# Kernel tuning notes

Measured on AMD Instinct MI355X. Metric: run time of the kernel, lower is better.

The kernel has to match this reference:

```python
import jax, jax.numpy as jnp
import numpy as np

N_NODES = 50000
IN_CH = 256
Z_DIM = 64
N_EDGES = 800000


def setup_inputs() -> dict:
    key = jax.random.key(0)
    k_x, k_e, k_wm, k_ws = jax.random.split(key, 4)
    x = jax.random.normal(k_x, (N_NODES, IN_CH), dtype=jnp.float32)
    edge_index = jax.random.randint(k_e, (2, N_EDGES), 0, N_NODES, dtype=jnp.int64)
    # Glorot-style init like PyG GCNConv
    scale = 1.0 / np.sqrt(IN_CH)
    W_mu = jax.random.uniform(k_wm, (IN_CH, Z_DIM), dtype=jnp.float32, minval=-scale, maxval=scale)
    W_logstd = jax.random.uniform(k_ws, (IN_CH, Z_DIM), dtype=jnp.float32, minval=-scale, maxval=scale)
    b_mu = jnp.zeros((Z_DIM,), dtype=jnp.float32)
    b_logstd = jnp.zeros((Z_DIM,), dtype=jnp.float32)
    return {"x": x, "edge_index": edge_index, "W_mu": W_mu, "b_mu": b_mu,
            "W_logstd": W_logstd, "b_logstd": b_logstd}


def _gcn_conv(x, W, b, src, dst, deg_inv_sqrt, num_nodes):
    # PyG GCNConv: out = D^{-1/2} (A + I) D^{-1/2} X W + b
    xw = x @ W                                   # [N, Z]
    norm = deg_inv_sqrt[src] * deg_inv_sqrt[dst]  # [E+N]
    msg = xw[src] * norm[:, None]                 # gather + scale, [E+N, Z]
    agg = jax.ops.segment_sum(msg, dst, num_segments=num_nodes)  # scatter-add
    return agg + b


def reference(x, edge_index, W_mu, b_mu, W_logstd, b_logstd):
    num_nodes = x.shape[0]
    loops = jnp.arange(num_nodes, dtype=edge_index.dtype)
    src = jnp.concatenate([edge_index[0], loops])
    dst = jnp.concatenate([edge_index[1], loops])
    # degree (with self loops) on target nodes, symmetric normalization
    deg = jax.ops.segment_sum(jnp.ones_like(dst, dtype=x.dtype), dst, num_segments=num_nodes)
    deg_inv_sqrt = jnp.where(deg > 0, jax.lax.rsqrt(jnp.maximum(deg, 1.0)), 0.0)
    mu = _gcn_conv(x, W_mu, b_mu, src, dst, deg_inv_sqrt, num_nodes)
    logstd = _gcn_conv(x, W_logstd, b_logstd, src, dst, deg_inv_sqrt, num_nodes)
    return (mu, logstd)
```

## Files before the change

### kernel.cpp

```cpp
#include <hip/hip_runtime.h>

#define N_NODES 50000
#define IN_CH   256
#define Z_DIM   64
#define N_EDGES 800000
#define CH2     128
#define NODE_OFF (N_NODES * Z_DIM)
#define NBLK    ((N_NODES + 255) / 256)
#define SEG     8
#define SEGN    50048
#define NBUCKET (SEG * SEGN)
#define CAP     16
#define ECHUNKS (N_EDGES / 256)
#define TM      128
#define GTILES  ((N_NODES + TM - 1) / TM)
#define NW      32768

typedef __bf16 bf16x8 __attribute__((ext_vector_type(8)));
typedef float  f32x4  __attribute__((ext_vector_type(4)));

__device__ __forceinline__ unsigned short f2bf(float f) {
    __bf16 h = (__bf16)f;
    unsigned short u;
    __builtin_memcpy(&u, &h, 2);
    return u;
}
__device__ __forceinline__ float bf_lo(unsigned w) { return __uint_as_float(w << 16); }
__device__ __forceinline__ float bf_hi(unsigned w) { return __uint_as_float(w & 0xFFFF0000u); }

__global__ void k_pre(int* __restrict__ cur8,
                      const float* __restrict__ Wmu, const float* __restrict__ Wls,
                      unsigned short* __restrict__ WbT) {
    int g = blockIdx.x * 256 + threadIdx.x;
    if (g < NBUCKET) cur8[g] = 0;
    int h = g - NBUCKET;
    if (h >= 0 && h < NW) {
        int n = h >> 8, k = h & 255;
        float v = (n < 64) ? Wmu[(size_t)k * 64 + n] : Wls[(size_t)k * 64 + (n - 64)];
        WbT[(size_t)n * 256 + k] = f2bf(v);
    }
}

__global__ __launch_bounds__(256) void k_scat(const int* __restrict__ src,
                                              const int* __restrict__ dst,
                                              int* __restrict__ cur8,
                                              unsigned short* __restrict__ pk2) {
    int e = blockIdx.x * 256 + threadIdx.x;
    int s = src[e];
    int d = dst[e];
    unsigned xcc;
    asm("s_getreg_b32 %0, hwreg(HW_REG_XCC_ID)" : "=s"(xcc));
    int idx = (int)(xcc & (SEG - 1)) * SEGN + d;
    int pos = __hip_atomic_fetch_add(&cur8[idx], 1, __ATOMIC_RELAXED,
                                     __HIP_MEMORY_SCOPE_WORKGROUP);
    if (pos < CAP) pk2[(size_t)idx * CAP + pos] = (unsigned short)s;
}

#define CSP2 136
__global__ __launch_bounds__(256, 2) void k_gemm(const float* __restrict__ x,
                                                 const unsigned short* __restrict__ WbT,
                                                 unsigned short* __restrict__ xwb) {
    __shared__ __align__(16) unsigned short As[TM * 256];
    const int tid = threadIdx.x;
    const int r0  = blockIdx.x * TM;

    {
        int row_l0 = tid >> 3;
        int cb     = (tid & 7) * 32;
#pragma unroll
        for (int r = 0; r < 4; ++r) {
            int row_l = r * 32 + row_l0;
            int row   = r0 + row_l;
            char* dpb = (char*)As + row_l * 512;
            unsigned cswz = (unsigned)((row_l & 7) << 4);
            if (row < N_NODES) {
                const float4* xp = (const float4*)(x + (size_t)row * IN_CH + cb);
#pragma unroll
                for (int i = 0; i < 4; ++i) {
                    float4 a = xp[2 * i];
                    float4 b = xp[2 * i + 1];
                    uint4 w;
                    w.x = (unsigned)f2bf(a.x) | ((unsigned)f2bf(a.y) << 16);
                    w.y = (unsigned)f2bf(a.z) | ((unsigned)f2bf(a.w) << 16);
                    w.z = (unsigned)f2bf(b.x) | ((unsigned)f2bf(b.y) << 16);
                    w.w = (unsigned)f2bf(b.z) | ((unsigned)f2bf(b.w) << 16);
                    *(uint4*)(dpb + (((unsigned)(cb * 2 + i * 16)) ^ cswz)) = w;
                }
            } else {
                uint4 z = make_uint4(0, 0, 0, 0);
#pragma unroll
                for (int i = 0; i < 4; ++i)
                    *(uint4*)(dpb + (((unsigned)(cb * 2 + i * 16)) ^ cswz)) = z;
            }
        }
    }
    __syncthreads();

    const int wv    = tid >> 6;
    const int lane  = tid & 63;
    const int m     = lane & 15;
    const int q     = lane >> 4;
    const int rbase = wv * 32;

    f32x4 acc[2][8] = {};
    const char* apb0 = (const char*)As + (rbase + m) * 512;
    const char* apb1 = apb0 + 16 * 512;
    const unsigned   sw  = (unsigned)((m & 7) << 4);
    const unsigned short* bp = WbT + (size_t)m * 256 + q * 8;

#pragma unroll
    for (int k0 = 0; k0 < IN_CH; k0 += 32) {
        unsigned off = ((unsigned)(q * 16 + 2 * k0)) ^ sw;
        bf16x8 a0 = *(const bf16x8*)(apb0 + off);
        bf16x8 a1 = *(const bf16x8*)(apb1 + off);
#pragma unroll
        for (int nt = 0; nt < 8; ++nt) {
            bf16x8 bf_ = *(const bf16x8*)(bp + (size_t)nt * 16 * 256 + k0);
            acc[0][nt] = __builtin_amdgcn_mfma_f32_16x16x32_bf16(a0, bf_, acc[0][nt], 0, 0, 0);
            acc[1][nt] = __builtin_amdgcn_mfma_f32_16x16x32_bf16(a1, bf_, acc[1][nt], 0, 0, 0);
        }
    }

    __syncthreads();
    {
        unsigned short* Css = As;
#pragma unroll
        for (int mi = 0; mi < 2; ++mi)
#pragma unroll
            for (int nt = 0; nt < 8; ++nt)
#pragma unroll
                for (int r = 0; r < 4; ++r)
                    Css[(rbase + mi * 16 + q * 4 + r) * CSP2 + nt * 16 + m] =
                        f2bf(acc[mi][nt][r]);
    }
    __syncthreads();
    {
        int row_l = tid >> 2;
        int c0    = (tid & 3) * 32;
#pragma unroll
        for (int rr = 0; rr < 2; ++rr) {
            int rl  = rr * 64 + row_l;
            int row = r0 + rl;
            if (row < N_NODES) {
                const uint4* cp = (const uint4*)(As + rl * CSP2 + c0);
                uint4 w0 = cp[0];
                uint4 w1 = cp[1];
                uint4 w2 = cp[2];
                uint4 w3 = cp[3];
                uint4* op = (uint4*)(xwb + (size_t)row * CH2 + c0);
                op[0] = w0; op[1] = w1; op[2] = w2; op[3] = w3;
            }
        }
    }
}

__global__ void k_dinv(const int* __restrict__ cur8, float* __restrict__ dinv) {
    int i = blockIdx.x * 256 + threadIdx.x;
    if (i >= N_NODES) return;
    int t = 1;
#pragma unroll
    for (int xg = 0; xg < SEG; ++xg) t += cur8[xg * SEGN + i];
    dinv[i] = rsqrtf((float)t);
}

#define PAIR(jj, pr)                                                          \
    if (2 * (jj) < cnt) {                                                     \
        int sa = (int)((pr) & 0xFFFFu);                                       \
        int sb = (int)((pr) >> 16);                                           \
        bool hb = (2 * (jj) + 1) < cnt;                                       \
        int sbe = hb ? sb : sa;                                               \
        float na = di * dinv[sa];                                             \
        float nb = hb ? di * dinv[sbe] : 0.f;                                 \
        const uint4 wa = *(const uint4*)(xwb + (size_t)sa * CH2 + cl * 8);    \
        const uint4 wb = *(const uint4*)(xwb + (size_t)sbe * CH2 + cl * 8);   \
        acc[0] += bf_lo(wa.x) * na + bf_lo(wb.x) * nb;                        \
        acc[1] += bf_hi(wa.x) * na + bf_hi(wb.x) * nb;                        \
        acc[2] += bf_lo(wa.y) * na + bf_lo(wb.y) * nb;                        \
        acc[3] += bf_hi(wa.y) * na + bf_hi(wb.y) * nb;                        \
        acc[4] += bf_lo(wa.z) * na + bf_lo(wb.z) * nb;                        \
        acc[5] += bf_hi(wa.z) * na + bf_hi(wb.z) * nb;                        \
        acc[6] += bf_lo(wa.w) * na + bf_lo(wb.w) * nb;                        \
        acc[7] += bf_hi(wa.w) * na + bf_hi(wb.w) * nb;                        \
    }

__global__ __launch_bounds__(256) void k_gather(const int* __restrict__ cur8,
                                                const unsigned short* __restrict__ pk2,
                                                const unsigned short* __restrict__ xwb,
                                                const float* __restrict__ dinv,
                                                const float* __restrict__ bmu,
                                                const float* __restrict__ bls,
                                                float* __restrict__ out) {
    const int i    = blockIdx.x * 4 + (threadIdx.x >> 6);
    const int lane = threadIdx.x & 63;
    const int q    = lane >> 4;
    const int cl   = lane & 15;

    float di = dinv[i];
    float acc[8] = {0.f, 0.f, 0.f, 0.f, 0.f, 0.f, 0.f, 0.f};
    if (q == 0) {
        float sq = di * di;
        uint4 w = *(const uint4*)(xwb + (size_t)i * CH2 + cl * 8);
        acc[0] = bf_lo(w.x) * sq; acc[1] = bf_hi(w.x) * sq;
        acc[2] = bf_lo(w.y) * sq; acc[3] = bf_hi(w.y) * sq;
        acc[4] = bf_lo(w.z) * sq; acc[5] = bf_hi(w.z) * sq;
        acc[6] = bf_lo(w.w) * sq; acc[7] = bf_hi(w.w) * sq;
    }

#pragma unroll
    for (int b = 0; b < 2; ++b) {
        const int idx = (q + b * 4) * SEGN + i;
        int cnt = cur8[idx];
        if (cnt > CAP) cnt = CAP;
        const uint4* pb = (const uint4*)(pk2 + (size_t)idx * CAP);
        const uint4 e0 = pb[0];
        const uint4 e1 = pb[1];
        PAIR(0, e0.x) PAIR(1, e0.y) PAIR(2, e0.z) PAIR(3, e0.w)
        PAIR(4, e1.x) PAIR(5, e1.y) PAIR(6, e1.z) PAIR(7, e1.w)
    }

#pragma unroll
    for (int k = 0; k < 8; ++k) {
        acc[k] += __shfl_xor(acc[k], 16);
        acc[k] += __shfl_xor(acc[k], 32);
    }

    if (lane < 16) {
        int c0 = cl * 8;
        const float* bb = (c0 < 64) ? (bmu + c0) : (bls + (c0 - 64));
        float4 b0 = *(const float4*)(bb + 0);
        float4 b1 = *(const float4*)(bb + 4);
        float* o = (c0 < 64) ? (out + (size_t)i * 64 + c0)
                             : (out + NODE_OFF + (size_t)i * 64 + (c0 - 64));
        *(float4*)(o + 0) = make_float4(acc[0] + b0.x, acc[1] + b0.y,
                                        acc[2] + b0.z, acc[3] + b0.w);
        *(float4*)(o + 4) = make_float4(acc[4] + b1.x, acc[5] + b1.y,
                                        acc[6] + b1.z, acc[7] + b1.w);
    }
}

extern "C" void kernel_launch(void* const* d_in, const int* in_sizes, int n_in,
                              void* d_out, int out_size, void* d_ws, size_t ws_size,
                              hipStream_t stream) {
    const float* x   = (const float*)d_in[0];
    const int*   ei  = (const int*)d_in[1];
    const float* Wmu = (const float*)d_in[2];
    const float* bmu = (const float*)d_in[3];
    const float* Wls = (const float*)d_in[4];
    const float* bls = (const float*)d_in[5];
    float* out = (float*)d_out;

    const int* src = ei;
    const int* dst = ei + N_EDGES;

    char* ws = (char*)d_ws;
    int*            cur8 = (int*)(ws + 0);
    float*          dinv = (float*)(ws + 1638400);
    unsigned short* WbT  = (unsigned short*)(ws + 1867776);
    unsigned short* pk2  = (unsigned short*)(ws + 2097152);
    unsigned short* xwb  = (unsigned short*)(ws + 16777216);

    k_pre<<<(NBUCKET + NW + 255) / 256, 256, 0, stream>>>(cur8, Wmu, Wls, WbT);
    k_scat<<<ECHUNKS, 256, 0, stream>>>(src, dst, cur8, pk2);
    k_gemm<<<GTILES, 256, 0, stream>>>(x, WbT, xwb);
    k_dinv<<<NBLK, 256, 0, stream>>>(cur8, dinv);
    k_gather<<<N_NODES / 4, 256, 0, stream>>>(cur8, pk2, xwb, dinv, bmu, bls, out);
}
```

Measured before the change: 204.1 us.

## Compact per-node neighbor lists and gather with 16 lanes per node

Extends the degree kernel so it also compacts the eight per-segment bucket lists of each node into one contiguous neighbor list with a count. The gather kernel then uses 16 lanes per node instead of 64, walks the compact list four neighbors at a time, and drops the cross-quarter shuffle reduction. This targets wasted lanes on empty bucket slots and the shuffle overhead. In exchange it adds a scalar per-thread copy pass with uncoalesced 2-byte loads and stores, plus extra workspace traffic.

```diff
diff --git a/kernel.cpp b/kernel.cpp
--- a/kernel.cpp
+++ b/kernel.cpp
@@ -11,6 +11,7 @@
 #define SEGN    50048
 #define NBUCKET (SEG * SEGN)
 #define CAP     16
+#define CAPN    64
 #define ECHUNKS (N_EDGES / 256)
 #define TM      128
 #define GTILES  ((N_NODES + TM - 1) / TM)
@@ -154,50 +155,52 @@
     }
 }
 
-__global__ void k_dinv(const int* __restrict__ cur8, float* __restrict__ dinv) {
+__global__ void k_dinv(const int* __restrict__ cur8,
+                       const unsigned short* __restrict__ pk2,
+                       float* __restrict__ dinv,
+                       unsigned short* __restrict__ plist,
+                       unsigned short* __restrict__ degc) {
     int i = blockIdx.x * 256 + threadIdx.x;
     if (i >= N_NODES) return;
-    int t = 1;
-#pragma unroll
-    for (int xg = 0; xg < SEG; ++xg) t += cur8[xg * SEGN + i];
-    dinv[i] = rsqrtf((float)t);
-}
-
-#define PAIR(jj, pr)                                                          \
-    if (2 * (jj) < cnt) {                                                     \
-        int sa = (int)((pr) & 0xFFFFu);                                       \
-        int sb = (int)((pr) >> 16);                                           \
-        bool hb = (2 * (jj) + 1) < cnt;                                       \
-        int sbe = hb ? sb : sa;                                               \
-        float na = di * dinv[sa];                                             \
-        float nb = hb ? di * dinv[sbe] : 0.f;                                 \
-        const uint4 wa = *(const uint4*)(xwb + (size_t)sa * CH2 + cl * 8);    \
-        const uint4 wb = *(const uint4*)(xwb + (size_t)sbe * CH2 + cl * 8);   \
-        acc[0] += bf_lo(wa.x) * na + bf_lo(wb.x) * nb;                        \
-        acc[1] += bf_hi(wa.x) * na + bf_hi(wb.x) * nb;                        \
-        acc[2] += bf_lo(wa.y) * na + bf_lo(wb.y) * nb;                        \
-        acc[3] += bf_hi(wa.y) * na + bf_hi(wb.y) * nb;                        \
-        acc[4] += bf_lo(wa.z) * na + bf_lo(wb.z) * nb;                        \
-        acc[5] += bf_hi(wa.z) * na + bf_hi(wb.z) * nb;                        \
-        acc[6] += bf_lo(wa.w) * na + bf_lo(wb.w) * nb;                        \
-        acc[7] += bf_hi(wa.w) * na + bf_hi(wb.w) * nb;                        \
-    }
-
-__global__ __launch_bounds__(256) void k_gather(const int* __restrict__ cur8,
-                                                const unsigned short* __restrict__ pk2,
+    int traw = 1;
+    int c[SEG];
+#pragma unroll
+    for (int s = 0; s < SEG; ++s) {
+        int cs = cur8[s * SEGN + i];
+        traw += cs;
+        c[s] = (cs > CAP) ? CAP : cs;
+    }
+    dinv[i] = rsqrtf((float)traw);
+
+    unsigned short* dp = plist + (size_t)i * CAPN;
+    int off = 0;
+#pragma unroll
+    for (int s = 0; s < SEG; ++s) {
+        const unsigned short* sp = pk2 + ((size_t)(s * SEGN + i)) * CAP;
+        int cc = c[s];
+        int lim = CAPN - off;
+        if (cc > lim) cc = lim;
+        for (int j = 0; j < cc; ++j) dp[off + j] = sp[j];
+        off += cc;
+    }
+    degc[i] = (unsigned short)off;
+}
+
+__global__ __launch_bounds__(256) void k_gather(const unsigned short* __restrict__ plist,
+                                                const unsigned short* __restrict__ degc,
                                                 const unsigned short* __restrict__ xwb,
                                                 const float* __restrict__ dinv,
                                                 const float* __restrict__ bmu,
                                                 const float* __restrict__ bls,
                                                 float* __restrict__ out) {
-    const int i    = blockIdx.x * 4 + (threadIdx.x >> 6);
-    const int lane = threadIdx.x & 63;
-    const int q    = lane >> 4;
-    const int cl   = lane & 15;
-
-    float di = dinv[i];
-    float acc[8] = {0.f, 0.f, 0.f, 0.f, 0.f, 0.f, 0.f, 0.f};
-    if (q == 0) {
+    const int i  = blockIdx.x * 16 + (threadIdx.x >> 4);
+    const int cl = threadIdx.x & 15;
+
+    const float di  = dinv[i];
+    const int   deg = degc[i];
+
+    float acc[8];
+    {
         float sq = di * di;
         uint4 w = *(const uint4*)(xwb + (size_t)i * CH2 + cl * 8);
         acc[0] = bf_lo(w.x) * sq; acc[1] = bf_hi(w.x) * sq;
@@ -206,25 +209,36 @@
         acc[6] = bf_lo(w.w) * sq; acc[7] = bf_hi(w.w) * sq;
     }
 
-#pragma unroll
-    for (int b = 0; b < 2; ++b) {
-        const int idx = (q + b * 4) * SEGN + i;
-        int cnt = cur8[idx];
-        if (cnt > CAP) cnt = CAP;
-        const uint4* pb = (const uint4*)(pk2 + (size_t)idx * CAP);
-        const uint4 e0 = pb[0];
-        const uint4 e1 = pb[1];
-        PAIR(0, e0.x) PAIR(1, e0.y) PAIR(2, e0.z) PAIR(3, e0.w)
-        PAIR(4, e1.x) PAIR(5, e1.y) PAIR(6, e1.z) PAIR(7, e1.w)
-    }
-
-#pragma unroll
-    for (int k = 0; k < 8; ++k) {
-        acc[k] += __shfl_xor(acc[k], 16);
-        acc[k] += __shfl_xor(acc[k], 32);
-    }
-
-    if (lane < 16) {
+    const unsigned short* lp = plist + (size_t)i * CAPN;
+    for (int j = 0; j < deg; j += 4) {
+        uint2 pe = *(const uint2*)(lp + j);
+        int s0 = (int)(pe.x & 0xFFFFu);
+        int s1 = (int)(pe.x >> 16);
+        int s2 = (int)(pe.y & 0xFFFFu);
+        int s3 = (int)(pe.y >> 16);
+        int rem = deg - j;
+        int e1 = (rem > 1) ? s1 : s0;
+        int e2 = (rem > 2) ? s2 : s0;
+        int e3 = (rem > 3) ? s3 : s0;
+        float n0 = di * dinv[s0];
+        float n1 = (rem > 1) ? di * dinv[e1] : 0.f;
+        float n2 = (rem > 2) ? di * dinv[e2] : 0.f;
+        float n3 = (rem > 3) ? di * dinv[e3] : 0.f;
+        const uint4 w0 = *(const uint4*)(xwb + (size_t)s0 * CH2 + cl * 8);
+        const uint4 w1 = *(const uint4*)(xwb + (size_t)e1 * CH2 + cl * 8);
+        const uint4 w2 = *(const uint4*)(xwb + (size_t)e2 * CH2 + cl * 8);
+        const uint4 w3 = *(const uint4*)(xwb + (size_t)e3 * CH2 + cl * 8);
+        acc[0] += bf_lo(w0.x) * n0 + bf_lo(w1.x) * n1 + bf_lo(w2.x) * n2 + bf_lo(w3.x) * n3;
+        acc[1] += bf_hi(w0.x) * n0 + bf_hi(w1.x) * n1 + bf_hi(w2.x) * n2 + bf_hi(w3.x) * n3;
+        acc[2] += bf_lo(w0.y) * n0 + bf_lo(w1.y) * n1 + bf_lo(w2.y) * n2 + bf_lo(w3.y) * n3;
+        acc[3] += bf_hi(w0.y) * n0 + bf_hi(w1.y) * n1 + bf_hi(w2.y) * n2 + bf_hi(w3.y) * n3;
+        acc[4] += bf_lo(w0.z) * n0 + bf_lo(w1.z) * n1 + bf_lo(w2.z) * n2 + bf_lo(w3.z) * n3;
+        acc[5] += bf_hi(w0.z) * n0 + bf_hi(w1.z) * n1 + bf_hi(w2.z) * n2 + bf_hi(w3.z) * n3;
+        acc[6] += bf_lo(w0.w) * n0 + bf_lo(w1.w) * n1 + bf_lo(w2.w) * n2 + bf_lo(w3.w) * n3;
+        acc[7] += bf_hi(w0.w) * n0 + bf_hi(w1.w) * n1 + bf_hi(w2.w) * n2 + bf_hi(w3.w) * n3;
+    }
+
+    {
         int c0 = cl * 8;
         const float* bb = (c0 < 64) ? (bmu + c0) : (bls + (c0 - 64));
         float4 b0 = *(const float4*)(bb + 0);
@@ -253,15 +267,17 @@
     const int* dst = ei + N_EDGES;
 
     char* ws = (char*)d_ws;
-    int*            cur8 = (int*)(ws + 0);
-    float*          dinv = (float*)(ws + 1638400);
-    unsigned short* WbT  = (unsigned short*)(ws + 1867776);
-    unsigned short* pk2  = (unsigned short*)(ws + 2097152);
-    unsigned short* xwb  = (unsigned short*)(ws + 16777216);
+    int*            cur8  = (int*)(ws + 0);
+    float*          dinv  = (float*)(ws + 1638400);
+    unsigned short* WbT   = (unsigned short*)(ws + 1867776);
+    unsigned short* pk2   = (unsigned short*)(ws + 2097152);
+    unsigned short* xwb   = (unsigned short*)(ws + 16777216);
+    unsigned short* plist = (unsigned short*)(ws + 29577216);
+    unsigned short* degc  = (unsigned short*)(ws + 35977216);
 
     k_pre<<<(NBUCKET + NW + 255) / 256, 256, 0, stream>>>(cur8, Wmu, Wls, WbT);
     k_scat<<<ECHUNKS, 256, 0, stream>>>(src, dst, cur8, pk2);
     k_gemm<<<GTILES, 256, 0, stream>>>(x, WbT, xwb);
-    k_dinv<<<NBLK, 256, 0, stream>>>(cur8, dinv);
-    k_gather<<<N_NODES / 4, 256, 0, stream>>>(cur8, pk2, xwb, dinv, bmu, bls, out);
-}
+    k_dinv<<<NBLK, 256, 0, stream>>>(cur8, pk2, dinv, plist, degc);
+    k_gather<<<N_NODES / 16, 256, 0, stream>>>(plist, degc, xwb, dinv, bmu, bls, out);
+}
```

Result: no change. 204.5 us (+0.2%).
